# Kernel tuning notes

Measured on AMD Instinct MI355X. Metric: run time of the kernel, lower is better.

## Reference

```python
import math
import jax, jax.numpy as jnp
import numpy as np

T = 4096
D_MODEL = 1024
NUM_HEADS = 16
HEAD_DIM = D_MODEL // NUM_HEADS


def setup_inputs() -> dict:
    key = jax.random.key(0)
    k_x, k_wqkv, k_wproj = jax.random.split(key, 3)
    # match eqx.nn.Linear init scale: U(-1/sqrt(in), 1/sqrt(in)); randn*small works too,
    # but keep magnitudes reasonable so softmax isn't saturated.
    s_in = 1.0 / math.sqrt(D_MODEL)
    x = jax.random.normal(k_x, (T, D_MODEL), dtype=jnp.float32)
    W_qkv = jax.random.normal(k_wqkv, (3 * D_MODEL, D_MODEL), dtype=jnp.float32) * s_in
    b_qkv = jnp.zeros((3 * D_MODEL,), dtype=jnp.float32)
    W_proj = jax.random.normal(k_wproj, (D_MODEL, D_MODEL), dtype=jnp.float32) * s_in
    b_proj = jnp.zeros((D_MODEL,), dtype=jnp.float32)
    return {"x": x, "W_qkv": W_qkv, "b_qkv": b_qkv, "W_proj": W_proj, "b_proj": b_proj}


def reference(x, W_qkv, b_qkv, W_proj, b_proj):
    T_, C = x.shape  # (seq, d_model)
    H, hd = NUM_HEADS, HEAD_DIM
    # c_attn: eqx Linear computes W @ x + b per token -> x @ W.T + b
    qkv = x @ W_qkv.T + b_qkv  # (T, 3C)
    q, k, v = jnp.split(qkv, 3, axis=1)
    # (T, C) -> (H, T, hd)
    q = q.reshape(T_, H, hd).swapaxes(0, 1)
    k = k.reshape(T_, H, hd).swapaxes(0, 1)
    v = v.reshape(T_, H, hd).swapaxes(0, 1)
    scores = jnp.einsum("htd,hsd->hts", q, k) / math.sqrt(hd)  # (H, T, T)
    causal = jnp.tril(jnp.ones((T_, T_), dtype=bool))
    scores = jnp.where(causal, scores, -jnp.inf)
    attn = jax.nn.softmax(scores, axis=-1)
    y = jnp.einsum("hts,hsd->htd", attn, v)  # (H, T, hd)
    y = y.swapaxes(0, 1).reshape(T_, C)
    y = y @ W_proj.T + b_proj
    return y
```

## Files before the change

### kernel.cpp

```cpp
#include <hip/hip_runtime.h>
#include <math.h>
#include <string.h>

#define T_SEQ 4096
#define DM 1024
#define NH 16
#define HD 64

typedef short s8v __attribute__((ext_vector_type(8)));
typedef float f4v __attribute__((ext_vector_type(4)));

__device__ inline unsigned short f2bf(float f) {
    unsigned u; memcpy(&u, &f, 4);
    u = u + 0x7fffu + ((u >> 16) & 1u);
    return (unsigned short)(u >> 16);
}

__device__ inline float bf2f(unsigned short s) {
    unsigned u = (unsigned)s << 16;
    float f; memcpy(&f, &u, 4);
    return f;
}

__device__ inline float exp2fn(float x) {
#if __has_builtin(__builtin_amdgcn_exp2f)
    return __builtin_amdgcn_exp2f(x);
#else
    return exp2f(x);
#endif
}

__device__ inline void gld_lds16(const void* g, void* l) {
    __builtin_amdgcn_global_load_lds(
        (const __attribute__((address_space(1))) void*)g,
        (__attribute__((address_space(3))) void*)l, 16, 0, 0);
}

__global__ __launch_bounds__(256)
void cvt3(const float* __restrict__ i0, unsigned short* __restrict__ o0, int n0,
          const float* __restrict__ i1, unsigned short* __restrict__ o1, int n1,
          const float* __restrict__ i2, unsigned short* __restrict__ o2, int n2) {
    int i = blockIdx.x * 256 + threadIdx.x;
    const float* in; unsigned short* out; int j;
    if (i < n0)           { in = i0; out = o0; j = i; }
    else if (i < n0 + n1) { in = i1; out = o1; j = i - n0; }
    else if (i < n0 + n1 + n2) { in = i2; out = o2; j = i - n0 - n1; }
    else return;
    const float4* p = (const float4*)(in + (size_t)j * 8);
    float4 a = p[0], b = p[1];
    unsigned short o[8] = {f2bf(a.x), f2bf(a.y), f2bf(a.z), f2bf(a.w),
                           f2bf(b.x), f2bf(b.y), f2bf(b.z), f2bf(b.w)};
    uint4 pk; memcpy(&pk, o, 16);
    *(uint4*)(out + (size_t)j * 8) = pk;
}

template<int MODE, int TN>
__global__ __launch_bounds__(256)
void gemm_bt_mfma(const unsigned short* __restrict__ A, const unsigned short* __restrict__ B,
                  const float* __restrict__ bias, void* __restrict__ Cout,
                  unsigned short* __restrict__ vT,
                  int M, int N, int K) {
    constexpr int NF = TN / 32;
    __shared__ __align__(16) short As[4096];
    __shared__ __align__(16) short Bs[TN * 32];
    const int tid = threadIdx.x;
    const int w = tid >> 6, lane = tid & 63;
    const int wr = w >> 1, wc = w & 1;
    const int m0 = blockIdx.y * 128, n0 = blockIdx.x * TN;

    const bool doA = (w < 2);
    const bool doStage = doA || ((w & 1) * 64 < TN);
    const unsigned short* src = doA ? A : B;
    const int rbase = (doA ? m0 : n0) + (w & 1) * 64;
    const unsigned short* gsrc = src + (size_t)(rbase + (lane & 15)) * K + ((lane >> 4) * 8);
    short* ldst = (doA ? As : Bs) + ((w & 1) * 4) * 512;

    f4v acc[4][NF];
    #pragma unroll
    for (int i = 0; i < 4; ++i)
        #pragma unroll
        for (int j = 0; j < NF; ++j) acc[i][j] = (f4v){0.f, 0.f, 0.f, 0.f};

    for (int k0 = 0; k0 < K; k0 += 32) {
        __syncthreads();
        if (doStage) {
            #pragma unroll
            for (int i = 0; i < 4; ++i)
                gld_lds16(gsrc + (size_t)(i * 16) * K + k0, ldst + i * 512);
        }
        __syncthreads();

        s8v af[4], bf[NF];
        #pragma unroll
        for (int i = 0; i < 4; ++i) af[i] = *(const s8v*)&As[((wr * 4 + i) * 64 + lane) * 8];
        #pragma unroll
        for (int j = 0; j < NF; ++j) bf[j] = *(const s8v*)&Bs[((wc * NF + j) * 64 + lane) * 8];
        #pragma unroll
        for (int i = 0; i < 4; ++i)
            #pragma unroll
            for (int j = 0; j < NF; ++j)
                acc[i][j] = __builtin_amdgcn_mfma_f32_16x16x32_bf16(af[i], bf[j], acc[i][j], 0, 0, 0);
    }

    const int l15 = lane & 15, quad = lane >> 4;
    float bj[NF];
    #pragma unroll
    for (int j = 0; j < NF; ++j) bj[j] = bias[n0 + wc * (TN / 2) + j * 16 + l15];

    if (MODE == 2 && n0 >= 2 * DM) {
        #pragma unroll
        for (int i = 0; i < 4; ++i) {
            int tb = m0 + wr * 64 + i * 16 + quad * 4;
            #pragma unroll
            for (int j = 0; j < NF; ++j) {
                int dg = n0 - 2 * DM + wc * (TN / 2) + j * 16 + l15;
                unsigned short o[4];
                #pragma unroll
                for (int rg = 0; rg < 4; ++rg) o[rg] = f2bf(acc[i][j][rg] + bj[j]);
                unsigned long long pk; memcpy(&pk, o, 8);
                *(unsigned long long*)&vT[(size_t)dg * T_SEQ + tb] = pk;
            }
        }
    } else {
        #pragma unroll
        for (int i = 0; i < 4; ++i) {
            #pragma unroll
            for (int rg = 0; rg < 4; ++rg) {
                int row = m0 + wr * 64 + i * 16 + quad * 4 + rg;
                #pragma unroll
                for (int j = 0; j < NF; ++j) {
                    int col = n0 + wc * (TN / 2) + j * 16 + l15;
                    float v = acc[i][j][rg] + bj[j];
                    if (MODE == 0) ((float*)Cout)[(size_t)row * N + col] = v;
                    else           ((unsigned short*)Cout)[(size_t)row * N + col] = f2bf(v);
                }
            }
        }
    }
}

__device__ __forceinline__ void soft_step(f4v* st, bool diag, int qloc, int quad, int l15,
                                          float& lr, short* pw) {
    const float C2  = 0.1803368851f;
    const float MC2 = 12.0f * 0.1803368851f;
    float sv[4][4];
    #pragma unroll
    for (int kb = 0; kb < 4; ++kb)
        #pragma unroll
        for (int rg = 0; rg < 4; ++rg) {
            float s = st[kb][rg];
            if (diag && (kb * 16 + quad * 4 + rg > qloc)) s = -3.0e38f;
            float t = exp2fn(fmaf(s, C2, -MC2));
            sv[kb][rg] = t;
            lr += t;
        }
    #pragma unroll
    for (int kb = 0; kb < 4; ++kb) {
        unsigned u0 = __float_as_uint(sv[kb][0]) + 0x8000u;
        unsigned u1 = __float_as_uint(sv[kb][1]) + 0x8000u;
        unsigned u2 = __float_as_uint(sv[kb][2]) + 0x8000u;
        unsigned u3 = __float_as_uint(sv[kb][3]) + 0x8000u;
        int2 v;
        v.x = (int)__builtin_amdgcn_perm(u1, u0, 0x07060302);
        v.y = (int)__builtin_amdgcn_perm(u3, u2, 0x07060302);
        int c = (kb >> 1) * 64 + ((kb & 1) * 2 + (quad >> 1)) * 16 + l15;
        c ^= ((c >> 3) & 7);
        *(int2*)&pw[c * 8 + (quad & 1) * 4] = v;
    }
}

__global__ __launch_bounds__(256, 2)
void attn_mfma5(const unsigned short* __restrict__ qkv,
                const unsigned short* __restrict__ vT,
                unsigned short* __restrict__ y0,
                unsigned short* __restrict__ y1,
                float* __restrict__ lsum) {
    const int b = blockIdx.x;
    const int par = b & 1;
    const int idx = b >> 1;
    const int h = idx & 15, a = idx >> 4;
    const int tid = threadIdx.x;
    const int w = tid >> 6, lane = tid & 63;
    const int quad = lane >> 4, l15 = lane & 15;
    const int cq = h * HD, hv = h * HD;
    const size_t rs = 3 * DM;
    unsigned short* ypar = par ? y1 : y0;
    float* lpar = lsum + ((size_t)par * NH + h) * T_SEQ;

    __shared__ short KB[2][4096];
    __shared__ short VTs[2][4096];
    __shared__ short QB[8192];
    __shared__ short PB[8][1024];

    for (int ph = 0; ph < 2; ++ph) {
        const int qt = ph ? (31 - a) : a;
        const int q0 = qt * 128;
        const int nk = qt + 1;
        const int kb0 = par * 64;

        __syncthreads();
        #pragma unroll
        for (int rr = 0; rr < 4; ++rr) {
            int ch = rr * 256 + tid;
            int qg = ch >> 7, hf = (ch >> 6) & 1, ln = ch & 63;
            gld_lds16(qkv + (size_t)(q0 + qg * 16 + (ln & 15)) * rs + cq + hf * 32 + ((ln >> 4) << 3),
                      &QB[(ch & ~63) * 8]);
        }
        #pragma unroll
        for (int rr = 0; rr < 2; ++rr) {
            int ch = rr * 256 + tid;
            int blk = ch >> 7, hf = (ch >> 6) & 1, ln = ch & 63;
            gld_lds16(qkv + (size_t)(kb0 + blk * 16 + (ln & 15)) * rs + DM + cq + hf * 32 + ((ln >> 4) << 3),
                      &KB[0][(ch & ~63) * 8]);
            gld_lds16(vT + (size_t)(hv + blk * 16 + (ln & 15)) * T_SEQ + kb0 + hf * 32 + ((ln >> 4) << 3),
                      &VTs[0][(ch & ~63) * 8]);
        }
        __syncthreads();

        s8v qf[2][2];
        #pragma unroll
        for (int g = 0; g < 2; ++g)
            #pragma unroll
            for (int hf = 0; hf < 2; ++hf)
                qf[g][hf] = *(const s8v*)&QB[((((g * 4 + w) * 2 + hf) * 64) + lane) * 8];

        f4v O0[4], O1[4];
        #pragma unroll
        for (int ob = 0; ob < 4; ++ob) {
            O0[ob] = (f4v){0.f, 0.f, 0.f, 0.f};
            O1[ob] = (f4v){0.f, 0.f, 0.f, 0.f};
        }
        float lr0 = 0.f, lr1 = 0.f;

        for (int i = 0; i < nk; ++i) {
            const int p = i & 1;
            const bool last = (i == nk - 1);
            const bool g0a = par ? !last : true;
            const bool m0 = (par == 0) && last;
            const bool m1 = (par == 1) && last;
            if (!last) {
                const int k1 = kb0 + (i + 1) * 128;
                #pragma unroll
                for (int rr = 0; rr < 2; ++rr) {
                    int ch = rr * 256 + tid;
                    int blk = ch >> 7, hf = (ch >> 6) & 1, ln = ch & 63;
                    gld_lds16(qkv + (size_t)(k1 + blk * 16 + (ln & 15)) * rs + DM + cq
                                  + hf * 32 + ((ln >> 4) << 3),
                              &KB[p ^ 1][(ch & ~63) * 8]);
                    gld_lds16(vT + (size_t)(hv + blk * 16 + (ln & 15)) * T_SEQ + k1
                                  + hf * 32 + ((ln >> 4) << 3),
                              &VTs[p ^ 1][(ch & ~63) * 8]);
                }
            }

            f4v st0[4], st1[4];
            #pragma unroll
            for (int kb = 0; kb < 4; ++kb) {
                s8v k0f = *(const s8v*)&KB[p][((kb * 2 + 0) * 64 + lane) * 8];
                s8v k1f = *(const s8v*)&KB[p][((kb * 2 + 1) * 64 + lane) * 8];
                f4v c1 = (f4v){0.f, 0.f, 0.f, 0.f};
                c1 = __builtin_amdgcn_mfma_f32_16x16x32_bf16(k0f, qf[1][0], c1, 0, 0, 0);
                c1 = __builtin_amdgcn_mfma_f32_16x16x32_bf16(k1f, qf[1][1], c1, 0, 0, 0);
                st1[kb] = c1;
                if (g0a) {
                    f4v c0 = (f4v){0.f, 0.f, 0.f, 0.f};
                    c0 = __builtin_amdgcn_mfma_f32_16x16x32_bf16(k0f, qf[0][0], c0, 0, 0, 0);
                    c0 = __builtin_amdgcn_mfma_f32_16x16x32_bf16(k1f, qf[0][1], c0, 0, 0, 0);
                    st0[kb] = c0;
                }
            }

            if (g0a) soft_step(st0, m0, w * 16 + l15, quad, l15, lr0, PB[w * 2 + 0]);
            soft_step(st1, m1, w * 16 + l15, quad, l15, lr1, PB[w * 2 + 1]);

            asm volatile("s_waitcnt lgkmcnt(0)" ::: "memory");
            int c0i = lane ^ ((lane >> 3) & 7);
            s8v pf10 = *(const s8v*)&PB[w * 2 + 1][c0i * 8];
            s8v pf11 = *(const s8v*)&PB[w * 2 + 1][(64 + c0i) * 8];
            s8v pf00, pf01;
            if (g0a) {
                pf00 = *(const s8v*)&PB[w * 2 + 0][c0i * 8];
                pf01 = *(const s8v*)&PB[w * 2 + 0][(64 + c0i) * 8];
            }

            #pragma unroll
            for (int ob = 0; ob < 4; ++ob) {
                s8v v0f = *(const s8v*)&VTs[p][((ob * 2 + 0) * 64 + lane) * 8];
                s8v v1f = *(const s8v*)&VTs[p][((ob * 2 + 1) * 64 + lane) * 8];
                O1[ob] = __builtin_amdgcn_mfma_f32_16x16x32_bf16(v0f, pf10, O1[ob], 0, 0, 0);
                O1[ob] = __builtin_amdgcn_mfma_f32_16x16x32_bf16(v1f, pf11, O1[ob], 0, 0, 0);
                if (g0a) {
                    O0[ob] = __builtin_amdgcn_mfma_f32_16x16x32_bf16(v0f, pf00, O0[ob], 0, 0, 0);
                    O0[ob] = __builtin_amdgcn_mfma_f32_16x16x32_bf16(v1f, pf01, O0[ob], 0, 0, 0);
                }
            }
            __syncthreads();
        }

        lr0 += __shfl_xor(lr0, 16); lr0 += __shfl_xor(lr0, 32);
        lr1 += __shfl_xor(lr1, 16); lr1 += __shfl_xor(lr1, 32);
        #pragma unroll
        for (int g = 0; g < 2; ++g) {
            const f4v* O = g ? O1 : O0;
            int qrow = q0 + g * 64 + w * 16 + l15;
            size_t ybase = (size_t)qrow * DM + cq;
            #pragma unroll
            for (int ob = 0; ob < 4; ++ob) {
                unsigned short o[4];
                #pragma unroll
                for (int rg = 0; rg < 4; ++rg) o[rg] = f2bf(O[ob][rg]);
                unsigned long long pk; memcpy(&pk, o, 8);
                *(unsigned long long*)&ypar[ybase + ob * 16 + quad * 4] = pk;
            }
            if (quad == 0) lpar[qrow] = g ? lr1 : lr0;
        }
    }
}

__global__ __launch_bounds__(256)
void attn_combine(const unsigned short* __restrict__ y0,
                  const unsigned short* __restrict__ y1,
                  const float* __restrict__ lsum,
                  unsigned short* __restrict__ yout) {
    int i = blockIdx.x * 256 + threadIdx.x;
    int t = i >> 7, d8 = i & 127;
    int h = d8 >> 3;
    float l = lsum[(size_t)h * T_SEQ + t] + lsum[((size_t)NH + h) * T_SEQ + t];
    float inv = 1.f / l;
    size_t off = (size_t)t * DM + d8 * 8;
    uint4 ua = *(const uint4*)(y0 + off);
    uint4 ub = *(const uint4*)(y1 + off);
    const unsigned short* pa = (const unsigned short*)&ua;
    const unsigned short* pb = (const unsigned short*)&ub;
    unsigned short o[8];
    #pragma unroll
    for (int k = 0; k < 8; ++k) o[k] = f2bf((bf2f(pa[k]) + bf2f(pb[k])) * inv);
    uint4 pk; memcpy(&pk, o, 16);
    *(uint4*)(yout + off) = pk;
}

extern "C" void kernel_launch(void* const* d_in, const int* in_sizes, int n_in,
                              void* d_out, int out_size, void* d_ws, size_t ws_size,
                              hipStream_t stream) {
    const float* x     = (const float*)d_in[0];
    const float* Wqkv  = (const float*)d_in[1];
    const float* bqkv  = (const float*)d_in[2];
    const float* Wproj = (const float*)d_in[3];
    const float* bproj = (const float*)d_in[4];
    float* out = (float*)d_out;

    char* ws = (char*)d_ws;
    unsigned short* qkvb  = (unsigned short*)(ws);
    unsigned short* yattb = (unsigned short*)(ws + (24u << 20));
    unsigned short* vTb   = (unsigned short*)(ws + (32u << 20));
    unsigned short* wprjb = (unsigned short*)(ws + (40u << 20));
    unsigned short* xb    = (unsigned short*)(ws + (42u << 20));
    unsigned short* wqkvb = (unsigned short*)(ws + (50u << 20));
    unsigned short* y0p   = (unsigned short*)(ws + (42u << 20));
    unsigned short* y1p   = (unsigned short*)(ws + (50u << 20));
    float*          lsum  = (float*)         (ws + (58u << 20));

    dim3 blk(256);
    {
        int n0 = T_SEQ * DM / 8, n1 = 3 * DM * DM / 8, n2 = DM * DM / 8;
        cvt3<<<dim3((n0 + n1 + n2 + 255) / 256), blk, 0, stream>>>(
            x, xb, n0, Wqkv, wqkvb, n1, Wproj, wprjb, n2);
    }
    gemm_bt_mfma<2, 128><<<dim3(3 * DM / 128, T_SEQ / 128), blk, 0, stream>>>(
        xb, wqkvb, bqkv, qkvb, vTb, T_SEQ, 3 * DM, DM);
    attn_mfma5<<<dim3(512), blk, 0, stream>>>(qkvb, vTb, y0p, y1p, lsum);
    attn_combine<<<dim3(T_SEQ * DM / 8 / 256), blk, 0, stream>>>(y0p, y1p, lsum, yattb);
    gemm_bt_mfma<0, 64><<<dim3(DM / 64, T_SEQ / 128), blk, 0, stream>>>(
        yattb, wprjb, bproj, out, nullptr, T_SEQ, DM, DM);
}
```

Measured before the change: 228.7 us.

## Split attention KV range three ways and split QKV output into Q/K buffers

Attention now splits each query tile's key range across three blocks (strided by 64-key tiles) instead of two, launching 768 blocks with a three-way partial-sum combine. LDS is cut by reusing the Q staging buffer for the P tiles, which allows three blocks per CU. The QKV GEMM writes Q and K to separate contiguous buffers with DM stride. The aim is more parallelism and better load balance, in exchange for an extra partial output to write and combine and an added barrier.

```diff
diff --git a/kernel.cpp b/kernel.cpp
--- a/kernel.cpp
+++ b/kernel.cpp
@@ -58,6 +58,7 @@
 __global__ __launch_bounds__(256)
 void gemm_bt_mfma(const unsigned short* __restrict__ A, const unsigned short* __restrict__ B,
                   const float* __restrict__ bias, void* __restrict__ Cout,
+                  unsigned short* __restrict__ qbuf, unsigned short* __restrict__ kbuf2,
                   unsigned short* __restrict__ vT,
                   int M, int N, int K) {
     constexpr int NF = TN / 32;
@@ -121,6 +122,21 @@
                 *(unsigned long long*)&vT[(size_t)dg * T_SEQ + tb] = pk;
             }
         }
+    } else if (MODE == 2) {
+        unsigned short* dst = (n0 < DM) ? qbuf : kbuf2;
+        const int nb = (n0 < DM) ? n0 : n0 - DM;
+        #pragma unroll
+        for (int i = 0; i < 4; ++i) {
+            #pragma unroll
+            for (int rg = 0; rg < 4; ++rg) {
+                int row = m0 + wr * 64 + i * 16 + quad * 4 + rg;
+                #pragma unroll
+                for (int j = 0; j < NF; ++j) {
+                    int col = nb + wc * (TN / 2) + j * 16 + l15;
+                    dst[(size_t)row * DM + col] = f2bf(acc[i][j][rg] + bj[j]);
+                }
+            }
+        }
     } else {
         #pragma unroll
         for (int i = 0; i < 4; ++i) {
@@ -130,9 +146,7 @@
                 #pragma unroll
                 for (int j = 0; j < NF; ++j) {
                     int col = n0 + wc * (TN / 2) + j * 16 + l15;
-                    float v = acc[i][j][rg] + bj[j];
-                    if (MODE == 0) ((float*)Cout)[(size_t)row * N + col] = v;
-                    else           ((unsigned short*)Cout)[(size_t)row * N + col] = f2bf(v);
+                    ((float*)Cout)[(size_t)row * N + col] = acc[i][j][rg] + bj[j];
                 }
             }
         }
@@ -169,51 +183,54 @@
     }
 }
 
-__global__ __launch_bounds__(256, 2)
-void attn_mfma5(const unsigned short* __restrict__ qkv,
+__global__ __launch_bounds__(256, 3)
+void attn_mfma6(const unsigned short* __restrict__ qb,
+                const unsigned short* __restrict__ kbf,
                 const unsigned short* __restrict__ vT,
                 unsigned short* __restrict__ y0,
                 unsigned short* __restrict__ y1,
+                unsigned short* __restrict__ y2,
                 float* __restrict__ lsum) {
     const int b = blockIdx.x;
-    const int par = b & 1;
-    const int idx = b >> 1;
+    const int par = b % 3;
+    const int idx = b / 3;
     const int h = idx & 15, a = idx >> 4;
     const int tid = threadIdx.x;
     const int w = tid >> 6, lane = tid & 63;
     const int quad = lane >> 4, l15 = lane & 15;
     const int cq = h * HD, hv = h * HD;
-    const size_t rs = 3 * DM;
-    unsigned short* ypar = par ? y1 : y0;
+    unsigned short* ypar = (par == 0) ? y0 : (par == 1) ? y1 : y2;
     float* lpar = lsum + ((size_t)par * NH + h) * T_SEQ;
 
     __shared__ short KB[2][4096];
     __shared__ short VTs[2][4096];
-    __shared__ short QB[8192];
-    __shared__ short PB[8][1024];
+    __shared__ short QP[8192];
 
     for (int ph = 0; ph < 2; ++ph) {
         const int qt = ph ? (31 - a) : a;
         const int q0 = qt * 128;
-        const int nk = qt + 1;
-        const int kb0 = par * 64;
+        const int kmax = 2 * qt + 1;
+        const int nk = (kmax >= par) ? (kmax - par) / 3 + 1 : 0;
+        const int kt0 = par * 64;
 
         __syncthreads();
         #pragma unroll
         for (int rr = 0; rr < 4; ++rr) {
             int ch = rr * 256 + tid;
             int qg = ch >> 7, hf = (ch >> 6) & 1, ln = ch & 63;
-            gld_lds16(qkv + (size_t)(q0 + qg * 16 + (ln & 15)) * rs + cq + hf * 32 + ((ln >> 4) << 3),
-                      &QB[(ch & ~63) * 8]);
-        }
-        #pragma unroll
-        for (int rr = 0; rr < 2; ++rr) {
-            int ch = rr * 256 + tid;
-            int blk = ch >> 7, hf = (ch >> 6) & 1, ln = ch & 63;
-            gld_lds16(qkv + (size_t)(kb0 + blk * 16 + (ln & 15)) * rs + DM + cq + hf * 32 + ((ln >> 4) << 3),
-                      &KB[0][(ch & ~63) * 8]);
-            gld_lds16(vT + (size_t)(hv + blk * 16 + (ln & 15)) * T_SEQ + kb0 + hf * 32 + ((ln >> 4) << 3),
-                      &VTs[0][(ch & ~63) * 8]);
+            gld_lds16(qb + (size_t)(q0 + qg * 16 + (ln & 15)) * DM + cq + hf * 32 + ((ln >> 4) << 3),
+                      &QP[(ch & ~63) * 8]);
+        }
+        if (nk > 0) {
+            #pragma unroll
+            for (int rr = 0; rr < 2; ++rr) {
+                int ch = rr * 256 + tid;
+                int blk = ch >> 7, hf = (ch >> 6) & 1, ln = ch & 63;
+                gld_lds16(kbf + (size_t)(kt0 + blk * 16 + (ln & 15)) * DM + cq + hf * 32 + ((ln >> 4) << 3),
+                          &KB[0][(ch & ~63) * 8]);
+                gld_lds16(vT + (size_t)(hv + blk * 16 + (ln & 15)) * T_SEQ + kt0 + hf * 32 + ((ln >> 4) << 3),
+                          &VTs[0][(ch & ~63) * 8]);
+            }
         }
         __syncthreads();
 
@@ -222,7 +239,8 @@
         for (int g = 0; g < 2; ++g)
             #pragma unroll
             for (int hf = 0; hf < 2; ++hf)
-                qf[g][hf] = *(const s8v*)&QB[((((g * 4 + w) * 2 + hf) * 64) + lane) * 8];
+                qf[g][hf] = *(const s8v*)&QP[((((g * 4 + w) * 2 + hf) * 64) + lane) * 8];
+        __syncthreads();
 
         f4v O0[4], O1[4];
         #pragma unroll
@@ -233,18 +251,18 @@
         float lr0 = 0.f, lr1 = 0.f;
 
         for (int i = 0; i < nk; ++i) {
+            const int kt = par + 3 * i;
             const int p = i & 1;
-            const bool last = (i == nk - 1);
-            const bool g0a = par ? !last : true;
-            const bool m0 = (par == 0) && last;
-            const bool m1 = (par == 1) && last;
-            if (!last) {
-                const int k1 = kb0 + (i + 1) * 128;
+            const bool g0a = (kt <= 2 * qt);
+            const bool m0 = (kt == 2 * qt);
+            const bool m1 = (kt == 2 * qt + 1);
+            if (i < nk - 1) {
+                const int k1 = kt0 + (i + 1) * 192;
                 #pragma unroll
                 for (int rr = 0; rr < 2; ++rr) {
                     int ch = rr * 256 + tid;
                     int blk = ch >> 7, hf = (ch >> 6) & 1, ln = ch & 63;
-                    gld_lds16(qkv + (size_t)(k1 + blk * 16 + (ln & 15)) * rs + DM + cq
+                    gld_lds16(kbf + (size_t)(k1 + blk * 16 + (ln & 15)) * DM + cq
                                   + hf * 32 + ((ln >> 4) << 3),
                               &KB[p ^ 1][(ch & ~63) * 8]);
                     gld_lds16(vT + (size_t)(hv + blk * 16 + (ln & 15)) * T_SEQ + k1
@@ -270,17 +288,18 @@
                 }
             }
 
-            if (g0a) soft_step(st0, m0, w * 16 + l15, quad, l15, lr0, PB[w * 2 + 0]);
-            soft_step(st1, m1, w * 16 + l15, quad, l15, lr1, PB[w * 2 + 1]);
+            short* PB = QP;
+            if (g0a) soft_step(st0, m0, w * 16 + l15, quad, l15, lr0, &PB[(w * 2 + 0) * 1024]);
+            soft_step(st1, m1, w * 16 + l15, quad, l15, lr1, &PB[(w * 2 + 1) * 1024]);
 
             asm volatile("s_waitcnt lgkmcnt(0)" ::: "memory");
             int c0i = lane ^ ((lane >> 3) & 7);
-            s8v pf10 = *(const s8v*)&PB[w * 2 + 1][c0i * 8];
-            s8v pf11 = *(const s8v*)&PB[w * 2 + 1][(64 + c0i) * 8];
+            s8v pf10 = *(const s8v*)&PB[(w * 2 + 1) * 1024 + c0i * 8];
+            s8v pf11 = *(const s8v*)&PB[(w * 2 + 1) * 1024 + (64 + c0i) * 8];
             s8v pf00, pf01;
             if (g0a) {
-                pf00 = *(const s8v*)&PB[w * 2 + 0][c0i * 8];
-                pf01 = *(const s8v*)&PB[w * 2 + 0][(64 + c0i) * 8];
+                pf00 = *(const s8v*)&PB[(w * 2 + 0) * 1024 + c0i * 8];
+                pf01 = *(const s8v*)&PB[(w * 2 + 0) * 1024 + (64 + c0i) * 8];
             }
 
             #pragma unroll
@@ -318,23 +337,29 @@
 }
 
 __global__ __launch_bounds__(256)
-void attn_combine(const unsigned short* __restrict__ y0,
-                  const unsigned short* __restrict__ y1,
-                  const float* __restrict__ lsum,
-                  unsigned short* __restrict__ yout) {
+void attn_combine3(const unsigned short* __restrict__ y0,
+                   const unsigned short* __restrict__ y1,
+                   const unsigned short* __restrict__ y2,
+                   const float* __restrict__ lsum,
+                   unsigned short* __restrict__ yout) {
     int i = blockIdx.x * 256 + threadIdx.x;
     int t = i >> 7, d8 = i & 127;
     int h = d8 >> 3;
-    float l = lsum[(size_t)h * T_SEQ + t] + lsum[((size_t)NH + h) * T_SEQ + t];
+    float l = lsum[(size_t)h * T_SEQ + t]
+            + lsum[((size_t)NH + h) * T_SEQ + t]
+            + lsum[((size_t)2 * NH + h) * T_SEQ + t];
     float inv = 1.f / l;
     size_t off = (size_t)t * DM + d8 * 8;
     uint4 ua = *(const uint4*)(y0 + off);
     uint4 ub = *(const uint4*)(y1 + off);
+    uint4 uc = *(const uint4*)(y2 + off);
     const unsigned short* pa = (const unsigned short*)&ua;
     const unsigned short* pb = (const unsigned short*)&ub;
+    const unsigned short* pc = (const unsigned short*)&uc;
     unsigned short o[8];
     #pragma unroll
-    for (int k = 0; k < 8; ++k) o[k] = f2bf((bf2f(pa[k]) + bf2f(pb[k])) * inv);
+    for (int k = 0; k < 8; ++k)
+        o[k] = f2bf((bf2f(pa[k]) + bf2f(pb[k]) + bf2f(pc[k])) * inv);
     uint4 pk; memcpy(&pk, o, 16);
     *(uint4*)(yout + off) = pk;
 }
@@ -350,15 +375,17 @@
     float* out = (float*)d_out;
 
     char* ws = (char*)d_ws;
-    unsigned short* qkvb  = (unsigned short*)(ws);
+    unsigned short* qbuf  = (unsigned short*)(ws);
+    unsigned short* kbuf  = (unsigned short*)(ws + ( 8u << 20));
+    unsigned short* vTb   = (unsigned short*)(ws + (16u << 20));
     unsigned short* yattb = (unsigned short*)(ws + (24u << 20));
-    unsigned short* vTb   = (unsigned short*)(ws + (32u << 20));
-    unsigned short* wprjb = (unsigned short*)(ws + (40u << 20));
-    unsigned short* xb    = (unsigned short*)(ws + (42u << 20));
-    unsigned short* wqkvb = (unsigned short*)(ws + (50u << 20));
-    unsigned short* y0p   = (unsigned short*)(ws + (42u << 20));
-    unsigned short* y1p   = (unsigned short*)(ws + (50u << 20));
-    float*          lsum  = (float*)         (ws + (58u << 20));
+    unsigned short* wprjb = (unsigned short*)(ws + (32u << 20));
+    float*          lsum  = (float*)         (ws + (34u << 20));
+    unsigned short* xb    = (unsigned short*)(ws + (35u << 20));
+    unsigned short* wqkvb = (unsigned short*)(ws + (43u << 20));
+    unsigned short* y0p   = (unsigned short*)(ws + (35u << 20));
+    unsigned short* y1p   = (unsigned short*)(ws + (43u << 20));
+    unsigned short* y2p   = (unsigned short*)(ws + (51u << 20));
 
     dim3 blk(256);
     {
@@ -367,9 +394,9 @@
             x, xb, n0, Wqkv, wqkvb, n1, Wproj, wprjb, n2);
     }
     gemm_bt_mfma<2, 128><<<dim3(3 * DM / 128, T_SEQ / 128), blk, 0, stream>>>(
-        xb, wqkvb, bqkv, qkvb, vTb, T_SEQ, 3 * DM, DM);
-    attn_mfma5<<<dim3(512), blk, 0, stream>>>(qkvb, vTb, y0p, y1p, lsum);
-    attn_combine<<<dim3(T_SEQ * DM / 8 / 256), blk, 0, stream>>>(y0p, y1p, lsum, yattb);
+        xb, wqkvb, bqkv, nullptr, qbuf, kbuf, vTb, T_SEQ, 3 * DM, DM);
+    attn_mfma6<<<dim3(768), blk, 0, stream>>>(qbuf, kbuf, vTb, y0p, y1p, y2p, lsum);
+    attn_combine3<<<dim3(T_SEQ * DM / 8 / 256), blk, 0, stream>>>(y0p, y1p, y2p, lsum, yattb);
     gemm_bt_mfma<0, 64><<<dim3(DM / 64, T_SEQ / 128), blk, 0, stream>>>(
-        yattb, wprjb, bproj, out, nullptr, T_SEQ, DM, DM);
-}
+        yattb, wprjb, bproj, out, nullptr, nullptr, nullptr, T_SEQ, DM, DM);
+}
```

New measurement: 231.9 us. About the same (+1.4%).
